# Kernel optimization log

Hardware: AMD Instinct MI355X
Metric: run time of the kernel (lower is better)

## Reference

```python
import jax, jax.numpy as jnp
import numpy as np


def _rotate_half(x):
    half = x.shape[-1] // 2
    x1, x2 = x[..., :half], x[..., half:]
    return jnp.concatenate([-x2, x1], axis=-1)


def setup_inputs() -> dict:
    key = jax.random.key(0)
    ks = jax.random.split(key, 7)
    B, T, D, H, Hd = 4, 2048, 1024, 16, 64
    x = jax.random.normal(ks[0], (B, T, D), dtype=jnp.float32)
    # RoPE tables (realistic: built from inv freqs)
    inv_freq = 1.0 / (10000.0 ** (jnp.arange(0, Hd, 2, dtype=jnp.float32) / Hd))
    pos = jnp.arange(T, dtype=jnp.float32)
    freqs = pos[:, None] * inv_freq[None, :]            # (T, Hd/2)
    emb = jnp.concatenate([freqs, freqs], axis=-1)       # (T, Hd)
    cos, sin = jnp.cos(emb), jnp.sin(emb)
    s = 1.0 / np.sqrt(D)
    w_q = jax.random.normal(ks[1], (D, D), dtype=jnp.float32) * s
    w_k = jax.random.normal(ks[2], (D, D), dtype=jnp.float32) * s
    w_v = jax.random.normal(ks[3], (D, D), dtype=jnp.float32) * s
    w_o = jax.random.normal(ks[4], (D, D), dtype=jnp.float32) * s
    return {"x": x, "cos": cos, "sin": sin, "w_q": w_q, "w_k": w_k, "w_v": w_v, "w_o": w_o}


def reference(x, cos, sin, w_q, w_k, w_v, w_o):
    B, T, D = x.shape
    H = 16
    Hd = D // H
    scale = Hd ** -0.5
    # nn.Linear(bias=False): y = x @ W.T
    q = (x @ w_q.T).reshape(B, T, H, Hd).transpose(0, 2, 1, 3)  # (B,H,T,Hd)
    k = (x @ w_k.T).reshape(B, T, H, Hd).transpose(0, 2, 1, 3)
    v = (x @ w_v.T).reshape(B, T, H, Hd).transpose(0, 2, 1, 3)
    c = cos[None, None, :, :]
    s = sin[None, None, :, :]
    q = q * c + _rotate_half(q) * s
    k = k * c + _rotate_half(k) * s
    scores = jnp.einsum('bhqd,bhkd->bhqk', q, k) * scale  # (B,H,T,T)
    causal = jnp.tril(jnp.ones((T, T), dtype=bool))
    scores = jnp.where(causal[None, None], scores, -jnp.inf)
    weights = jax.nn.softmax(scores, axis=-1)
    out = jnp.einsum('bhqk,bhkd->bhqd', weights, v)
    out = out.transpose(0, 2, 1, 3).reshape(B, T, D)
    return out @ w_o.T
```

## Files before the change

### kernel.cpp

```cpp
#include <hip/hip_runtime.h>
#include <stdint.h>

typedef __attribute__((ext_vector_type(8))) __bf16 bf16x8;
typedef __attribute__((ext_vector_type(4))) float floatx4;


__device__ __forceinline__ unsigned short f2bf(float f) {
    unsigned int u = __float_as_uint(f);
    u += 0x7FFFu + ((u >> 16) & 1u);
    return (unsigned short)(u >> 16);
}
__device__ __forceinline__ unsigned int pack2bf(float lo, float hi) {
    return (unsigned int)f2bf(lo) | ((unsigned int)f2bf(hi) << 16);
}
__device__ __forceinline__ unsigned int packtrunc(float lo, float hi) {
    return __builtin_amdgcn_perm(__float_as_uint(hi), __float_as_uint(lo), 0x07060302u);
}

__device__ __forceinline__ void gl_lds16(const void* g, void* l) {
    __builtin_amdgcn_global_load_lds(
        (const __attribute__((address_space(1))) void*)g,
        (__attribute__((address_space(3))) void*)l, 16, 0, 0);
}


__global__ void cvt_all(const float* __restrict__ x,  const float* __restrict__ wq,
                        const float* __restrict__ wk, const float* __restrict__ wv,
                        const float* __restrict__ wo,
                        unsigned short* __restrict__ xb,  unsigned short* __restrict__ wqb,
                        unsigned short* __restrict__ wkb, unsigned short* __restrict__ wvb,
                        unsigned short* __restrict__ wob) {
    int i = blockIdx.x * blockDim.x + threadIdx.x;
    const float* in; unsigned short* out; int idx;
    if (i < 2097152) { in = x; out = xb; idx = i; }
    else {
        int j = i - 2097152; int wsel = j >> 18; idx = j & 262143;
        in  = (wsel == 0) ? wq  : (wsel == 1) ? wk  : (wsel == 2) ? wv  : wo;
        out = (wsel == 0) ? wqb : (wsel == 1) ? wkb : (wsel == 2) ? wvb : wob;
    }
    float4 v = ((const float4*)in)[idx];
    ushort4 o;
    o.x = f2bf(v.x); o.y = f2bf(v.y); o.z = f2bf(v.z); o.w = f2bf(v.w);
    ((ushort4*)out)[idx] = o;
}


template<int MODE>
__global__ __launch_bounds__(256, 2)
void gemm_bt(const unsigned short* __restrict__ A,
             const unsigned short* __restrict__ Wq,
             const unsigned short* __restrict__ Wk,
             const float* __restrict__ cosp,
             const float* __restrict__ sinp,
             unsigned short* __restrict__ outq,
             unsigned short* __restrict__ outk,
             unsigned short* __restrict__ outvt,
             float* __restrict__ outf)
{
    constexpr int K = 1024;
    __shared__ __align__(16) unsigned short As[128 * 32];
    __shared__ __align__(16) unsigned short Bs[128 * 32];

    const int t    = threadIdx.x;
    const int w    = t >> 6;
    const int lane = t & 63;
    const int c    = lane & 15;
    const int quad = lane >> 4;
    const int wr   = w >> 1, wc = w & 1;

    const int m0 = blockIdx.x * 128;
    int which, n0;
    const unsigned short* W;
    if constexpr (MODE == 0) {
        which = blockIdx.y >> 3;
        n0    = (blockIdx.y & 7) * 128;
        W     = which ? Wk : Wq;
    } else {
        which = 0;
        n0    = blockIdx.y * 128;
        W     = Wq;
    }

    const int srow = t >> 2;
    const int scol = (t & 3) * 8;
    const unsigned short* ga0 = A + (size_t)(m0 + srow) * K + scol;
    const unsigned short* ga1 = A + (size_t)(m0 + srow + 64) * K + scol;
    const unsigned short* gb0 = W + (size_t)(n0 + srow) * K + scol;
    const unsigned short* gb1 = W + (size_t)(n0 + srow + 64) * K + scol;
    void* lA0 = (char*)As + t * 16;
    void* lA1 = (char*)As + 4096 + t * 16;
    void* lB0 = (char*)Bs + t * 16;
    void* lB1 = (char*)Bs + 4096 + t * 16;

    floatx4 acc[4][4] = {};

    const int arow = wr * 64;
    const int brow = wc * 64;

    for (int k0 = 0; k0 < K; k0 += 32) {
        __syncthreads();
        gl_lds16(ga0 + k0, lA0);
        gl_lds16(ga1 + k0, lA1);
        gl_lds16(gb0 + k0, lB0);
        gl_lds16(gb1 + k0, lB1);
        __syncthreads();
        bf16x8 af[4], bfr[4];
        #pragma unroll
        for (int mi = 0; mi < 4; mi++)
            af[mi] = *(const bf16x8*)&As[(arow + mi * 16 + c) * 32 + quad * 8];
        #pragma unroll
        for (int ni = 0; ni < 4; ni++)
            bfr[ni] = *(const bf16x8*)&Bs[(brow + ni * 16 + c) * 32 + quad * 8];
        if constexpr (MODE == 2) {
            #pragma unroll
            for (int mi = 0; mi < 4; mi++)
                #pragma unroll
                for (int ni = 0; ni < 4; ni++)
                    acc[mi][ni] = __builtin_amdgcn_mfma_f32_16x16x32_bf16(
                        af[mi], bfr[ni], acc[mi][ni], 0, 0, 0);
        } else {
            #pragma unroll
            for (int mi = 0; mi < 4; mi++)
                #pragma unroll
                for (int ni = 0; ni < 4; ni++)
                    acc[mi][ni] = __builtin_amdgcn_mfma_f32_16x16x32_bf16(
                        bfr[ni], af[mi], acc[mi][ni], 0, 0, 0);
        }
    }

    if constexpr (MODE == 1) {
        #pragma unroll
        for (int mi = 0; mi < 4; mi++) {
            int m = m0 + wr * 64 + mi * 16 + c;
            #pragma unroll
            for (int ni = 0; ni < 4; ni++) {
                int n = n0 + wc * 64 + ni * 16 + quad * 4;
                *(floatx4*)&outf[(size_t)m * 1024 + n] = acc[mi][ni];
            }
        }
    } else if constexpr (MODE == 2) {
        const int hh = (n0 + wc * 64) >> 6;
        #pragma unroll
        for (int mi = 0; mi < 4; mi++) {
            int t0 = m0 + wr * 64 + mi * 16 + quad * 4;
            int b = t0 >> 11, tt0 = t0 & 2047;
            #pragma unroll
            for (int ni = 0; ni < 4; ni++) {
                int d = ni * 16 + c;
                uint2 pk;
                pk.x = pack2bf(acc[mi][ni][0], acc[mi][ni][1]);
                pk.y = pack2bf(acc[mi][ni][2], acc[mi][ni][3]);
                *(uint2*)&outvt[((size_t)((b * 16 + hh) * 64 + d)) * 2048 + tt0] = pk;
            }
        }
    } else {
        const int hh = (n0 + wc * 64) >> 6;
        unsigned short* dst = which ? outk : outq;
        const float scale = which ? 1.0f : (0.125f * 1.44269504088896f);
        #pragma unroll
        for (int mi = 0; mi < 4; mi++) {
            int m = m0 + wr * 64 + mi * 16 + c;
            int b = m >> 11, tt = m & 2047;
            size_t obase = ((size_t)(b * 16 + hh) * 2048 + tt) * 64;
            #pragma unroll
            for (int ni = 0; ni < 4; ni++) {
                int d0 = ni * 16 + quad * 4;
                float4 cv = *(const float4*)&cosp[tt * 64 + d0];
                float4 sv = *(const float4*)&sinp[tt * 64 + d0];
                float ca[4] = {cv.x, cv.y, cv.z, cv.w};
                float sa[4] = {sv.x, sv.y, sv.z, sv.w};
                float vq[4];
                #pragma unroll
                for (int r = 0; r < 4; r++) {
                    float pr  = acc[mi][ni ^ 2][r];
                    float rot = (ni & 2) ? pr : -pr;
                    vq[r] = (acc[mi][ni][r] * ca[r] + rot * sa[r]) * scale;
                }
                uint2 pk;
                pk.x = pack2bf(vq[0], vq[1]);
                pk.y = pack2bf(vq[2], vq[3]);
                *(uint2*)&dst[obase + d0] = pk;
            }
        }
    }
}

__global__ __launch_bounds__(256)
void flash_attn(const unsigned short* __restrict__ Q,
                const unsigned short* __restrict__ Kg,
                const unsigned short* __restrict__ Vt,
                unsigned short* __restrict__ O)
{
    __shared__ __align__(16) unsigned short Ks[2][64 * 64];
    __shared__ __align__(16) unsigned short Vs[2][64 * 64];
    __shared__ __align__(16) unsigned short Ps[4 * 16 * 64];

    const int t    = threadIdx.x;
    const int w    = t >> 6;
    const int lane = t & 63;
    const int c    = lane & 15;
    const int quad = lane >> 4;

    const int bh = blockIdx.x;
    const int b  = bh >> 4, h = bh & 15;

    const unsigned short* qp = Q  + (size_t)bh * 2048 * 64;
    const unsigned short* kp = Kg + (size_t)bh * 2048 * 64;
    const unsigned short* vp = Vt + (size_t)bh * 64 * 2048;

    const int srow = t >> 3;
    const int sj   = (t & 7) ^ (srow & 7);
    unsigned short* pw = Ps + w * (16 * 64);

    for (int pp = 0; pp < 2; pp++) {
        const int qi = pp ? (31 - (int)blockIdx.y) : (int)blockIdx.y;
        const int q0 = qi * 64;
        const int qb = q0 + w * 16;

        bf16x8 qf[2];
        #pragma unroll
        for (int dc = 0; dc < 2; dc++)
            qf[dc] = *(const bf16x8*)&qp[(size_t)(qb + c) * 64 + dc * 32 + quad * 8];

        floatx4 o[4] = {};
        float lpart = 0.f;

        __syncthreads();
        #pragma unroll
        for (int ch = 0; ch < 2; ch++) {
            int kr = ch * 32 + srow;
            gl_lds16(kp + (size_t)kr * 64 + sj * 8, (char*)&Ks[0][0] + ch * 4096 + t * 16);
            gl_lds16(vp + (size_t)kr * 2048 + sj * 8, (char*)&Vs[0][0] + ch * 4096 + t * 16);
        }

        const int iters = qi + 1;
        for (int it = 0; it < iters; it++) {
            const int cur = it & 1;
            const int kt0 = it * 64;
            __syncthreads();
            if (it + 1 < iters) {
                const int kt1 = kt0 + 64;
                #pragma unroll
                for (int ch = 0; ch < 2; ch++) {
                    int kr = ch * 32 + srow;
                    gl_lds16(kp + (size_t)(kt1 + kr) * 64 + sj * 8,
                             (char*)&Ks[cur ^ 1][0] + ch * 4096 + t * 16);
                    gl_lds16(vp + (size_t)kr * 2048 + kt1 + sj * 8,
                             (char*)&Vs[cur ^ 1][0] + ch * 4096 + t * 16);
                }
            }
            const unsigned short* KsC = &Ks[cur][0];
            const unsigned short* VsC = &Vs[cur][0];

            floatx4 s[4] = {};
            #pragma unroll
            for (int dc = 0; dc < 2; dc++) {
                const int phys = (dc * 4 + quad) ^ (c & 7);
                #pragma unroll
                for (int mt = 0; mt < 4; mt++) {
                    bf16x8 kb = *(const bf16x8*)&KsC[(mt * 16 + c) * 64 + phys * 8];
                    s[mt] = __builtin_amdgcn_mfma_f32_16x16x32_bf16(kb, qf[dc], s[mt], 0, 0, 0);
                }
            }

            if (it == iters - 1) {
                #pragma unroll
                for (int mt = 0; mt < 4; mt++) {
                    int keyb = kt0 + mt * 16 + quad * 4;
                    #pragma unroll
                    for (int r = 0; r < 4; r++)
                        if (keyb + r > qb + c) s[mt][r] = -1e30f;
                }
            }

            uint2 pk[4];
            #pragma unroll
            for (int mt = 0; mt < 4; mt++) {
                float p0 = __builtin_amdgcn_exp2f(s[mt][0]);
                float p1 = __builtin_amdgcn_exp2f(s[mt][1]);
                float p2 = __builtin_amdgcn_exp2f(s[mt][2]);
                float p3 = __builtin_amdgcn_exp2f(s[mt][3]);
                lpart += (p0 + p1) + (p2 + p3);
                pk[mt].x = packtrunc(p0, p1);
                pk[mt].y = packtrunc(p2, p3);
            }

            #pragma unroll
            for (int mt = 0; mt < 4; mt++) {
                int blk = (mt * 2 + (quad >> 1)) ^ (c & 7);
                *(uint2*)&pw[c * 64 + blk * 8 + (quad & 1) * 4] = pk[mt];
            }

            #pragma unroll
            for (int kc = 0; kc < 2; kc++) {
                const int phys = (kc * 4 + quad) ^ (c & 7);
                bf16x8 ap = *(const bf16x8*)&pw[c * 64 + phys * 8];
                #pragma unroll
                for (int ni = 0; ni < 4; ni++) {
                    bf16x8 vb = *(const bf16x8*)&VsC[(ni * 16 + c) * 64 + phys * 8];
                    o[ni] = __builtin_amdgcn_mfma_f32_16x16x32_bf16(ap, vb, o[ni], 0, 0, 0);
                }
            }
        }

        float l = lpart;
        l += __shfl_xor(l, 16);
        l += __shfl_xor(l, 32);
        float li = __builtin_amdgcn_rcpf(l);
        #pragma unroll
        for (int r = 0; r < 4; r++) {
            float linv = __shfl(li, quad * 4 + r);
            int qrow = qb + quad * 4 + r;
            size_t base = ((size_t)(b * 2048 + qrow)) * 1024 + h * 64;
            #pragma unroll
            for (int ni = 0; ni < 4; ni++)
                O[base + ni * 16 + c] = f2bf(o[ni][r] * linv);
        }
    }
}


extern "C" void kernel_launch(void* const* d_in, const int* in_sizes, int n_in,
                              void* d_out, int out_size, void* d_ws, size_t ws_size,
                              hipStream_t stream) {
    const float* x    = (const float*)d_in[0];
    const float* cosp = (const float*)d_in[1];
    const float* sinp = (const float*)d_in[2];
    const float* wq   = (const float*)d_in[3];
    const float* wk   = (const float*)d_in[4];
    const float* wv   = (const float*)d_in[5];
    const float* wo   = (const float*)d_in[6];

    char* ws = (char*)d_ws;
    const size_t MB = 1024 * 1024;
    unsigned short* xb   = (unsigned short*)(ws + 0);
    unsigned short* attn = (unsigned short*)(ws + 0);
    unsigned short* wqb  = (unsigned short*)(ws + 16 * MB);
    unsigned short* wkb  = (unsigned short*)(ws + 18 * MB);
    unsigned short* wvb  = (unsigned short*)(ws + 20 * MB);
    unsigned short* wob  = (unsigned short*)(ws + 22 * MB);
    unsigned short* qbuf = (unsigned short*)(ws + 24 * MB);
    unsigned short* kbuf = (unsigned short*)(ws + 40 * MB);
    unsigned short* vtb  = (unsigned short*)(ws + 56 * MB);

    cvt_all<<<dim3(12288), 256, 0, stream>>>(x, wq, wk, wv, wo,
                                             xb, wqb, wkb, wvb, wob);

    gemm_bt<0><<<dim3(64, 16), 256, 0, stream>>>(xb, wqb, wkb, cosp, sinp,
                                                 qbuf, kbuf, nullptr, nullptr);
    gemm_bt<2><<<dim3(64, 8), 256, 0, stream>>>(xb, wvb, nullptr, nullptr, nullptr,
                                                nullptr, nullptr, vtb, nullptr);

    flash_attn<<<dim3(64, 16), 256, 0, stream>>>(qbuf, kbuf, vtb, attn);

    gemm_bt<1><<<dim3(64, 8), 256, 0, stream>>>(attn, wob, nullptr, nullptr, nullptr,
                                                nullptr, nullptr, nullptr, (float*)d_out);
}
```

Baseline: 265.1 us.

## Keep softmax P in registers via permlane swaps and compute row sums with MFMA

```diff
diff --git a/kernel.cpp b/kernel.cpp
--- a/kernel.cpp
+++ b/kernel.cpp
@@ -193,7 +193,6 @@
 {
     __shared__ __align__(16) unsigned short Ks[2][64 * 64];
     __shared__ __align__(16) unsigned short Vs[2][64 * 64];
-    __shared__ __align__(16) unsigned short Ps[4 * 16 * 64];
 
     const int t    = threadIdx.x;
     const int w    = t >> 6;
@@ -210,112 +209,113 @@
 
     const int srow = t >> 3;
     const int sj   = (t & 7) ^ (srow & 7);
-    unsigned short* pw = Ps + w * (16 * 64);
-
-    for (int pp = 0; pp < 2; pp++) {
-        const int qi = pp ? (31 - (int)blockIdx.y) : (int)blockIdx.y;
-        const int q0 = qi * 64;
-        const int qb = q0 + w * 16;
-
-        bf16x8 qf[2];
-        #pragma unroll
-        for (int dc = 0; dc < 2; dc++)
-            qf[dc] = *(const bf16x8*)&qp[(size_t)(qb + c) * 64 + dc * 32 + quad * 8];
-
-        floatx4 o[4] = {};
-        float lpart = 0.f;
-
+
+    const int qi = 31 - (int)blockIdx.y;
+    const int q0 = qi * 64;
+    const int qb = q0 + w * 16;
+
+    bf16x8 qf[2];
+    #pragma unroll
+    for (int dc = 0; dc < 2; dc++)
+        qf[dc] = *(const bf16x8*)&qp[(size_t)(qb + c) * 64 + dc * 32 + quad * 8];
+
+    union { unsigned short us[8]; bf16x8 v; } one8;
+    #pragma unroll
+    for (int j = 0; j < 8; j++) one8.us[j] = 0x3F80;
+
+    floatx4 o[4] = {};
+    floatx4 lacc = {};
+
+    #pragma unroll
+    for (int ch = 0; ch < 2; ch++) {
+        int kr = ch * 32 + srow;
+        gl_lds16(kp + (size_t)kr * 64 + sj * 8, (char*)&Ks[0][0] + ch * 4096 + t * 16);
+        gl_lds16(vp + (size_t)kr * 2048 + sj * 8, (char*)&Vs[0][0] + ch * 4096 + t * 16);
+    }
+
+    const int iters = qi + 1;
+    for (int it = 0; it < iters; it++) {
+        const int cur = it & 1;
+        const int kt0 = it * 64;
         __syncthreads();
-        #pragma unroll
-        for (int ch = 0; ch < 2; ch++) {
-            int kr = ch * 32 + srow;
-            gl_lds16(kp + (size_t)kr * 64 + sj * 8, (char*)&Ks[0][0] + ch * 4096 + t * 16);
-            gl_lds16(vp + (size_t)kr * 2048 + sj * 8, (char*)&Vs[0][0] + ch * 4096 + t * 16);
-        }
-
-        const int iters = qi + 1;
-        for (int it = 0; it < iters; it++) {
-            const int cur = it & 1;
-            const int kt0 = it * 64;
-            __syncthreads();
-            if (it + 1 < iters) {
-                const int kt1 = kt0 + 64;
+        if (it + 1 < iters) {
+            const int kt1 = kt0 + 64;
+            #pragma unroll
+            for (int ch = 0; ch < 2; ch++) {
+                int kr = ch * 32 + srow;
+                gl_lds16(kp + (size_t)(kt1 + kr) * 64 + sj * 8,
+                         (char*)&Ks[cur ^ 1][0] + ch * 4096 + t * 16);
+                gl_lds16(vp + (size_t)kr * 2048 + kt1 + sj * 8,
+                         (char*)&Vs[cur ^ 1][0] + ch * 4096 + t * 16);
+            }
+        }
+        const unsigned short* KsC = &Ks[cur][0];
+        const unsigned short* VsC = &Vs[cur][0];
+
+        floatx4 s[4] = {};
+        #pragma unroll
+        for (int dc = 0; dc < 2; dc++) {
+            const int phys = (dc * 4 + quad) ^ (c & 7);
+            #pragma unroll
+            for (int mt = 0; mt < 4; mt++) {
+                bf16x8 kb = *(const bf16x8*)&KsC[(mt * 16 + c) * 64 + phys * 8];
+                s[mt] = __builtin_amdgcn_mfma_f32_16x16x32_bf16(kb, qf[dc], s[mt], 0, 0, 0);
+            }
+        }
+
+        if (it == iters - 1) {
+            #pragma unroll
+            for (int mt = 0; mt < 4; mt++) {
+                int keyb = kt0 + mt * 16 + quad * 4;
                 #pragma unroll
-                for (int ch = 0; ch < 2; ch++) {
-                    int kr = ch * 32 + srow;
-                    gl_lds16(kp + (size_t)(kt1 + kr) * 64 + sj * 8,
-                             (char*)&Ks[cur ^ 1][0] + ch * 4096 + t * 16);
-                    gl_lds16(vp + (size_t)kr * 2048 + kt1 + sj * 8,
-                             (char*)&Vs[cur ^ 1][0] + ch * 4096 + t * 16);
-                }
-            }
-            const unsigned short* KsC = &Ks[cur][0];
-            const unsigned short* VsC = &Vs[cur][0];
-
-            floatx4 s[4] = {};
-            #pragma unroll
-            for (int dc = 0; dc < 2; dc++) {
-                const int phys = (dc * 4 + quad) ^ (c & 7);
-                #pragma unroll
-                for (int mt = 0; mt < 4; mt++) {
-                    bf16x8 kb = *(const bf16x8*)&KsC[(mt * 16 + c) * 64 + phys * 8];
-                    s[mt] = __builtin_amdgcn_mfma_f32_16x16x32_bf16(kb, qf[dc], s[mt], 0, 0, 0);
-                }
-            }
-
-            if (it == iters - 1) {
-                #pragma unroll
-                for (int mt = 0; mt < 4; mt++) {
-                    int keyb = kt0 + mt * 16 + quad * 4;
-                    #pragma unroll
-                    for (int r = 0; r < 4; r++)
-                        if (keyb + r > qb + c) s[mt][r] = -1e30f;
-                }
-            }
-
-            uint2 pk[4];
-            #pragma unroll
-            for (int mt = 0; mt < 4; mt++) {
-                float p0 = __builtin_amdgcn_exp2f(s[mt][0]);
-                float p1 = __builtin_amdgcn_exp2f(s[mt][1]);
-                float p2 = __builtin_amdgcn_exp2f(s[mt][2]);
-                float p3 = __builtin_amdgcn_exp2f(s[mt][3]);
-                lpart += (p0 + p1) + (p2 + p3);
-                pk[mt].x = packtrunc(p0, p1);
-                pk[mt].y = packtrunc(p2, p3);
-            }
-
-            #pragma unroll
-            for (int mt = 0; mt < 4; mt++) {
-                int blk = (mt * 2 + (quad >> 1)) ^ (c & 7);
-                *(uint2*)&pw[c * 64 + blk * 8 + (quad & 1) * 4] = pk[mt];
-            }
-
-            #pragma unroll
-            for (int kc = 0; kc < 2; kc++) {
-                const int phys = (kc * 4 + quad) ^ (c & 7);
-                bf16x8 ap = *(const bf16x8*)&pw[c * 64 + phys * 8];
-                #pragma unroll
-                for (int ni = 0; ni < 4; ni++) {
-                    bf16x8 vb = *(const bf16x8*)&VsC[(ni * 16 + c) * 64 + phys * 8];
-                    o[ni] = __builtin_amdgcn_mfma_f32_16x16x32_bf16(ap, vb, o[ni], 0, 0, 0);
-                }
-            }
-        }
-
-        float l = lpart;
-        l += __shfl_xor(l, 16);
-        l += __shfl_xor(l, 32);
-        float li = __builtin_amdgcn_rcpf(l);
-        #pragma unroll
-        for (int r = 0; r < 4; r++) {
-            float linv = __shfl(li, quad * 4 + r);
-            int qrow = qb + quad * 4 + r;
-            size_t base = ((size_t)(b * 2048 + qrow)) * 1024 + h * 64;
-            #pragma unroll
-            for (int ni = 0; ni < 4; ni++)
-                O[base + ni * 16 + c] = f2bf(o[ni][r] * linv);
-        }
+                for (int r = 0; r < 4; r++)
+                    if (keyb + r > qb + c) s[mt][r] = -1e30f;
+            }
+        }
+
+        uint2 pk[4];
+        #pragma unroll
+        for (int mt = 0; mt < 4; mt++) {
+            float p0 = __builtin_amdgcn_exp2f(s[mt][0]);
+            float p1 = __builtin_amdgcn_exp2f(s[mt][1]);
+            float p2 = __builtin_amdgcn_exp2f(s[mt][2]);
+            float p3 = __builtin_amdgcn_exp2f(s[mt][3]);
+            pk[mt].x = packtrunc(p0, p1);
+            pk[mt].y = packtrunc(p2, p3);
+        }
+
+        #pragma unroll
+        for (int kc = 0; kc < 2; kc++) {
+            unsigned int x0 = pk[2 * kc].x;
+            unsigned int x1 = pk[2 * kc].y;
+            unsigned int x2 = pk[2 * kc + 1].x;
+            unsigned int x3 = pk[2 * kc + 1].y;
+            asm("v_permlane32_swap_b32 %0, %1" : "+v"(x0), "+v"(x2));
+            asm("v_permlane32_swap_b32 %0, %1" : "+v"(x1), "+v"(x3));
+            asm("v_permlane16_swap_b32 %0, %1" : "+v"(x0), "+v"(x2));
+            asm("v_permlane16_swap_b32 %0, %1" : "+v"(x1), "+v"(x3));
+            union { unsigned int u[4]; bf16x8 v; } ap;
+            ap.u[0] = x0; ap.u[1] = x1; ap.u[2] = x2; ap.u[3] = x3;
+
+            lacc = __builtin_amdgcn_mfma_f32_16x16x32_bf16(ap.v, one8.v, lacc, 0, 0, 0);
+
+            const int phys = (kc * 4 + quad) ^ (c & 7);
+            #pragma unroll
+            for (int ni = 0; ni < 4; ni++) {
+                bf16x8 vb = *(const bf16x8*)&VsC[(ni * 16 + c) * 64 + phys * 8];
+                o[ni] = __builtin_amdgcn_mfma_f32_16x16x32_bf16(ap.v, vb, o[ni], 0, 0, 0);
+            }
+        }
+    }
+
+    #pragma unroll
+    for (int r = 0; r < 4; r++) {
+        float linv = __builtin_amdgcn_rcpf(lacc[r]);
+        int qrow = qb + quad * 4 + r;
+        size_t base = ((size_t)(b * 2048 + qrow)) * 1024 + h * 64;
+        #pragma unroll
+        for (int ni = 0; ni < 4; ni++)
+            O[base + ni * 16 + c] = f2bf(o[ni][r] * linv);
     }
 }
 
@@ -351,7 +351,7 @@
     gemm_bt<2><<<dim3(64, 8), 256, 0, stream>>>(xb, wvb, nullptr, nullptr, nullptr,
                                                 nullptr, nullptr, vtb, nullptr);
 
-    flash_attn<<<dim3(64, 16), 256, 0, stream>>>(qbuf, kbuf, vtb, attn);
+    flash_attn<<<dim3(64, 32), 256, 0, stream>>>(qbuf, kbuf, vtb, attn);
 
     gemm_bt<1><<<dim3(64, 8), 256, 0, stream>>>(attn, wob, nullptr, nullptr, nullptr,
                                                 nullptr, nullptr, nullptr, (float*)d_out);
```

Result: faster. 255.0 us (-3.8%).
